# Kernel optimization log

Hardware: AMD Instinct MI355X
Metric: run time of the kernel (lower is better)

Reference implementation:

```python
import jax, jax.numpy as jnp
import numpy as np

WH, WW = 16, 16
NUM_HEADS = 16
DIM = 1024
BATCH = 64
SEQ = WH * WW + 1  # 257, includes cls token
NUM_REL = (2 * WH - 1) * (2 * WW - 1) + 3  # 964


def _make_rel_pos_index(wh, ww):
    # BEiT relative position index construction (intended semantics of the torch code)
    coords = np.stack(np.meshgrid(np.arange(wh), np.arange(ww), indexing='ij'))  # [2, wh, ww]
    flat = coords.reshape(2, -1)  # [2, wh*ww]
    rel = flat[:, :, None] - flat[:, None, :]  # [2, N-1, N-1]
    rel = rel.transpose(1, 2, 0).astype(np.int64)
    rel[:, :, 0] += wh - 1
    rel[:, :, 1] += ww - 1
    rel[:, :, 0] *= 2 * ww - 1
    num_rel = (2 * wh - 1) * (2 * ww - 1) + 3
    idx = np.zeros((wh * ww + 1, wh * ww + 1), dtype=np.int32)
    idx[1:, 1:] = rel.sum(-1)
    idx[0, :] = num_rel - 3  # cls-to-token
    idx[:, 0] = num_rel - 2  # token-to-cls
    idx[0, 0] = num_rel - 1  # cls-to-cls
    return idx


def setup_inputs() -> dict:
    key = jax.random.key(0)
    ks = jax.random.split(key, 7)
    return {
        'x': jax.random.normal(ks[0], (BATCH, SEQ, DIM), dtype=jnp.float32),
        'qkv_weight': jax.random.normal(ks[1], (3 * DIM, DIM), dtype=jnp.float32) * 0.02,
        'query_bias': jax.random.normal(ks[2], (DIM,), dtype=jnp.float32) * 0.02,
        'value_bias': jax.random.normal(ks[3], (DIM,), dtype=jnp.float32) * 0.02,
        'rel_pos_bias_table': jax.random.normal(ks[4], (NUM_REL, NUM_HEADS), dtype=jnp.float32) * 0.02,
        'proj_weight': jax.random.normal(ks[5], (DIM, DIM), dtype=jnp.float32) * 0.02,
        'proj_bias': jax.random.normal(ks[6], (DIM,), dtype=jnp.float32) * 0.02,
        'rel_pos_index': jnp.asarray(_make_rel_pos_index(WH, WW)),
    }


def reference(x, qkv_weight, query_bias, value_bias, rel_pos_bias_table,
              proj_weight, proj_bias, rel_pos_index):
    B, N, C = x.shape
    H = rel_pos_bias_table.shape[-1]
    D = qkv_weight.shape[0] // 3 // H
    scale = D ** -0.5
    # qkv bias: (q_bias, zeros, v_bias) as in the torch module
    qkv_bias = jnp.concatenate([query_bias, jnp.zeros_like(value_bias), value_bias])
    qkv = x @ qkv_weight.T + qkv_bias  # [B, N, 3*H*D]
    qkv = qkv.reshape(B, N, 3, H, D).transpose(2, 0, 3, 1, 4)  # [3, B, H, N, D]
    q, k, v = qkv[0] * scale, qkv[1], qkv[2]
    attn = jnp.einsum('bhqd,bhkd->bhqk', q, k)  # [B, H, N, N]
    bias = rel_pos_bias_table[rel_pos_index]  # [N, N, H]
    attn = attn + bias.transpose(2, 0, 1)[None]  # add per-head bias
    attn = jax.nn.softmax(attn, axis=-1)
    out = jnp.einsum('bhqk,bhkd->bhqd', attn, v)  # [B, H, N, D]
    out = out.transpose(0, 2, 1, 3).reshape(B, N, H * D)
    return out @ proj_weight.T + proj_bias
```

## Files before the change

kernel.cpp:

```cpp
#include <hip/hip_runtime.h>


typedef unsigned short u16;
typedef __attribute__((ext_vector_type(8))) short bf16x8;
typedef __attribute__((ext_vector_type(4))) float f32x4;

#define MFMA16(a, b, c) __builtin_amdgcn_mfma_f32_16x16x32_bf16(a, b, c, 0, 0, 0)
#define GLDS16(g, l)                                                           \
  __builtin_amdgcn_global_load_lds(                                            \
      (const __attribute__((address_space(1))) void*)(g),                      \
      (__attribute__((address_space(3))) void*)(l), 16, 0, 0)

#define QOFF 0
#define KOFF 16842752
#define VTOFF 33685504
#define VTP 264

__device__ __forceinline__ u16 f2bf(float f) {
  unsigned u = __builtin_bit_cast(unsigned, f);
  u += 0x7FFFu + ((u >> 16) & 1u);
  return (u16)(u >> 16);
}
__device__ __forceinline__ unsigned pack2(float a, float b) {
  return (unsigned)f2bf(a) | ((unsigned)f2bf(b) << 16);
}

__global__ __launch_bounds__(256) void cvt_bf16(const float* __restrict__ in,
                                                u16* __restrict__ out, int n4) {
  int i = blockIdx.x * 256 + threadIdx.x;
  if (i < n4) {
    float4 v = ((const float4*)in)[i];
    uint2 o;
    o.x = pack2(v.x, v.y);
    o.y = pack2(v.z, v.w);
    ((uint2*)out)[i] = o;
  }
}

__global__ __launch_bounds__(256) void bias_pre(const float* __restrict__ tab,
                                                const int* __restrict__ idx,
                                                float* __restrict__ out) {
  int t = blockIdx.x * 256 + threadIdx.x;
  if (t < 66049) {
    int id = idx[t];
    const float* row = tab + (size_t)id * 16;
#pragma unroll
    for (int h = 0; h < 16; h++)
      out[(size_t)h * 66049 + t] = row[h] * 1.4426950408889634f;
  }
}


#define GEMM_PROLOG(M_, K_)                                                    \
  __shared__ __align__(16) u16 SMEM[8192];                                     \
  u16* const As = SMEM;                                                        \
  u16* const Bs = SMEM + 4096;                                                 \
  const int M = (M_), K = (K_);                                                \
  const int tid = threadIdx.x;                                                 \
  const int lane = tid & 63, wave = tid >> 6;                                  \
  const int quad = lane >> 4, l15 = lane & 15;                                 \
  const int wr = (wave >> 1) * 64, wc = (wave & 1) * 64;                       \
  const int m0 = blockIdx.y * 128, n0 = blockIdx.x * 128;                      \
  const int sgk = (((tid & 3) ^ ((tid >> 3) & 3))) * 8;  \
  const int fo = ((quad ^ ((l15 >> 1) & 3))) * 8;         \
  int ar0 = m0 + (tid >> 2); if (ar0 > M - 1) ar0 = M - 1;                     \
  int ar1 = m0 + 64 + (tid >> 2); if (ar1 > M - 1) ar1 = M - 1;                \
  const u16* pa0 = A + (size_t)ar0 * K + sgk;                                  \
  const u16* pa1 = A + (size_t)ar1 * K + sgk;                                  \
  const u16* pb0 = B + (size_t)(n0 + (tid >> 2)) * K + sgk;                    \
  const u16* pb1 = pb0 + (size_t)64 * K;                                       \
  f32x4 acc[4][4];                                                             \
  _Pragma("unroll") for (int i = 0; i < 4; i++)                                \
  _Pragma("unroll") for (int j = 0; j < 4; j++)                                \
      acc[i][j] = (f32x4){0.f, 0.f, 0.f, 0.f};                                 \
  for (int k0 = 0; k0 < K; k0 += 32) {                                         \
    __syncthreads();                                                           \
    GLDS16(pa0 + k0, As + tid * 8);                                            \
    GLDS16(pa1 + k0, As + 2048 + tid * 8);                                     \
    GLDS16(pb0 + k0, Bs + tid * 8);                                            \
    GLDS16(pb1 + k0, Bs + 2048 + tid * 8);                                     \
    __syncthreads();                                                           \
    bf16x8 bfr[4];                                                             \
    _Pragma("unroll") for (int t = 0; t < 4; t++)                              \
        bfr[t] = *(const bf16x8*)(Bs + (wc + t * 16 + l15) * 32 + fo);         \
    _Pragma("unroll") for (int i = 0; i < 4; i++) {                            \
      bf16x8 afr = *(const bf16x8*)(As + (wr + i * 16 + l15) * 32 + fo);       \
      _Pragma("unroll") for (int j = 0; j < 4; j++)                            \
          acc[i][j] = MFMA16(afr, bfr[j], acc[i][j]);                          \
    }                                                                          \
  }

__global__ __launch_bounds__(256, 4) void gemm_qkv(
    const u16* __restrict__ A, const u16* __restrict__ B,
    const float* __restrict__ qbias, const float* __restrict__ vbias,
    u16* __restrict__ C) {
  GEMM_PROLOG(16448, 1024)
  if (n0 >= 2048) {
    u16* const T = SMEM;
    for (int p = 0; p < 2; p++) {
      __syncthreads();
      if ((wave & 1) == p) {
#pragma unroll
        for (int j = 0; j < 4; j++) {
          int cl = j * 16 + l15;
          int rem = (n0 + wc + j * 16 + l15) & 1023;
          float vb_ = vbias[rem];
          int swz = (cl & 15) << 3;
#pragma unroll
          for (int i = 0; i < 4; i++) {
            int rlb = wr + i * 16 + quad * 4;
#pragma unroll
            for (int rr = 0; rr < 2; rr++) {
              unsigned pk = pack2(acc[i][j][rr * 2] + vb_,
                                  acc[i][j][rr * 2 + 1] + vb_);
              *(unsigned*)(T + cl * 128 + ((rlb + rr * 2) ^ swz)) = pk;
            }
          }
        }
      }
      __syncthreads();
#pragma unroll
      for (int cc = 0; cc < 16; cc++) {
        int cl = cc * 4 + wave;
        int rem = (n0 + p * 64 + cl) & 1023;
        int h = rem >> 6, d = rem & 63;
        size_t cb = (size_t)VTOFF + ((size_t)h * 64 + d) * VTP;
        int swz = (cl & 15) << 3;
#pragma unroll
        for (int half = 0; half < 2; half++) {
          int rl = half * 64 + lane;
          u16 val = T[cl * 128 + (rl ^ swz)];
          int m = m0 + rl;
          if (m < M) {
            unsigned bb2 = (unsigned)m / 257u;
            unsigned nn2 = (unsigned)m - bb2 * 257u;
            C[cb + (size_t)bb2 * (16 * 64 * VTP) + nn2] = val;
          }
        }
      }
    }
  } else {
#pragma unroll
    for (int i = 0; i < 4; i++) {
#pragma unroll
      for (int r = 0; r < 4; r++) {
        int row = m0 + wr + i * 16 + quad * 4 + r;
        if (row < M) {
          unsigned bb = (unsigned)row / 257u;
          unsigned nn = (unsigned)row - bb * 257u;
#pragma unroll
          for (int j = 0; j < 4; j++) {
            int c = n0 + wc + j * 16 + l15;
            int which = c >> 10, rem = c & 1023;
            float bias = (which == 0) ? qbias[rem] : 0.f;
            float v = acc[i][j][r] + bias;
            if (which == 0) v *= 0.18033688011112042f;
            int h = rem >> 6, d = rem & 63;
            size_t dst = (size_t)which * 16842752 +
                         (size_t)(bb * 16 + h) * 16448 + (size_t)nn * 64 + d;
            C[dst] = f2bf(v);
          }
        }
      }
    }
  }
}

__global__ __launch_bounds__(256, 4) void gemm_proj(
    const u16* __restrict__ A, const u16* __restrict__ B,
    const float* __restrict__ pbias, float* __restrict__ C) {
  GEMM_PROLOG(16448, 1024)
#pragma unroll
  for (int i = 0; i < 4; i++) {
#pragma unroll
    for (int r = 0; r < 4; r++) {
      int row = m0 + wr + i * 16 + quad * 4 + r;
      if (row < M) {
#pragma unroll
        for (int j = 0; j < 4; j++) {
          int c = n0 + wc + j * 16 + l15;
          C[(size_t)row * 1024 + c] = acc[i][j][r] + pbias[c];
        }
      }
    }
  }
}

__global__ __launch_bounds__(256, 3) void attn_fused(
    const u16* __restrict__ qkv, const float* __restrict__ biasT,
    u16* __restrict__ out) {
  __shared__ __align__(16) u16 KVs[96 * 72];
  __shared__ __align__(16) u16 Ps[4 * 16 * 104];
  const int bx = blockIdx.x;
  const int qt = bx % 5, bh = bx / 5;
  const int b = bh >> 4, h = bh & 15;
  const int tid = threadIdx.x, lane = tid & 63, wave = tid >> 6;
  const int quad = lane >> 4, l15 = lane & 15;
  const u16* qg = qkv + QOFF + (size_t)bh * 16448;
  const u16* kg = qkv + KOFF + (size_t)bh * 16448;
  const u16* vtg = qkv + VTOFF + (size_t)bh * (64 * VTP);

  int qra = qt * 64 + wave * 16 + l15;
  if (qra > 256) qra = 256;
  const bf16x8 aq0 = *(const bf16x8*)(qg + (size_t)qra * 64 + quad * 8);
  const bf16x8 aq1 = *(const bf16x8*)(qg + (size_t)qra * 64 + 32 + quad * 8);

  const int qbase = qt * 64 + wave * 16 + quad * 4;
  const float* bb = biasT + (size_t)h * 66049;
  f32x4 s[18];
#pragma unroll
  for (int r = 0; r < 4; r++) {
    int qr = qbase + r;
    if (qr > 256) qr = 256;
    const float* brow = bb + (size_t)qr * 257;
#pragma unroll
    for (int t = 0; t < 18; t++) {
      int kc = t * 16 + l15;
      s[t][r] = (kc < 257) ? brow[kc] : -3e38f;
    }
  }

  const bf16x8 zv = {0, 0, 0, 0, 0, 0, 0, 0};
  for (int ck = 0; ck < 3; ck++) {
    __syncthreads();
#pragma unroll
    for (int it = 0; it < 3; it++) {
      int g = it * 256 + tid;
      int row = g >> 3, col = (g & 7) * 8;
      int gr = ck * 96 + row;
      bf16x8 kv = (gr < 257) ? *(const bf16x8*)(kg + (size_t)gr * 64 + col) : zv;
      *(bf16x8*)(KVs + row * 72 + col) = kv;
    }
    __syncthreads();
#pragma unroll
    for (int nt = 0; nt < 6; nt++) {
      bf16x8 b0 = *(const bf16x8*)(KVs + (nt * 16 + l15) * 72 + quad * 8);
      bf16x8 b1 = *(const bf16x8*)(KVs + (nt * 16 + l15) * 72 + 32 + quad * 8);
      int t = ck * 6 + nt;
      s[t] = MFMA16(aq0, b0, s[t]);
      s[t] = MFMA16(aq1, b1, s[t]);
    }
  }

  float inv[4];
#pragma unroll
  for (int r = 0; r < 4; r++) {
    float m = -3e38f;
#pragma unroll
    for (int t = 0; t < 18; t++) m = fmaxf(m, s[t][r]);
    m = fmaxf(m, __shfl_xor(m, 1));
    m = fmaxf(m, __shfl_xor(m, 2));
    m = fmaxf(m, __shfl_xor(m, 4));
    m = fmaxf(m, __shfl_xor(m, 8));
    float sum = 0.f;
#pragma unroll
    for (int t = 0; t < 18; t++) {
      float p = __builtin_amdgcn_exp2f(s[t][r] - m);
      s[t][r] = p;
      sum += p;
    }
    sum += __shfl_xor(sum, 1);
    sum += __shfl_xor(sum, 2);
    sum += __shfl_xor(sum, 4);
    sum += __shfl_xor(sum, 8);
    inv[r] = 1.f / sum;
  }

  u16* Pw = Ps + wave * (16 * 104);
  f32x4 o[4];
#pragma unroll
  for (int nt = 0; nt < 4; nt++) o[nt] = (f32x4){0.f, 0.f, 0.f, 0.f};
  for (int ck = 0; ck < 3; ck++) {
    __syncthreads();
#pragma unroll
    for (int it = 0; it < 3; it++) {
      int g = it * 256 + tid;
      int row = g / 12, c = (g % 12) * 8;
      bf16x8 v = *(const bf16x8*)(vtg + (size_t)row * VTP + ck * 96 + c);
      *(bf16x8*)(KVs + row * 104 + c) = v;
    }
#pragma unroll
    for (int nt = 0; nt < 6; nt++) {
      int t = ck * 6 + nt;
#pragma unroll
      for (int r = 0; r < 4; r++)
        Pw[(quad * 4 + r) * 104 + nt * 16 + l15] = f2bf(s[t][r]);
    }
    __syncthreads();
#pragma unroll
    for (int ks = 0; ks < 3; ks++) {
      bf16x8 ap = *(const bf16x8*)(Pw + l15 * 104 + ks * 32 + quad * 8);
#pragma unroll
      for (int nt = 0; nt < 4; nt++) {
        bf16x8 bv =
            *(const bf16x8*)(KVs + (nt * 16 + l15) * 104 + ks * 32 + quad * 8);
        o[nt] = MFMA16(ap, bv, o[nt]);
      }
    }
  }

#pragma unroll
  for (int nt = 0; nt < 4; nt++) {
    int d = nt * 16 + l15;
#pragma unroll
    for (int r = 0; r < 4; r++) {
      int qr = qbase + r;
      if (qr < 257)
        out[((size_t)b * 257 + qr) * 1024 + h * 64 + d] =
            f2bf(o[nt][r] * inv[r]);
    }
  }
}

extern "C" void kernel_launch(void* const* d_in, const int* in_sizes, int n_in,
                              void* d_out, int out_size, void* d_ws,
                              size_t ws_size, hipStream_t stream) {
  const float* x = (const float*)d_in[0];
  const float* qkvw = (const float*)d_in[1];
  const float* qb = (const float*)d_in[2];
  const float* vb = (const float*)d_in[3];
  const float* tab = (const float*)d_in[4];
  const float* pw = (const float*)d_in[5];
  const float* pb = (const float*)d_in[6];
  const int* rpi = (const int*)d_in[7];

  char* ws = (char*)d_ws;
  u16* qkvbuf = (u16*)ws;
  u16* xbuf = (u16*)(ws + 101974016);
  float* biasb = (float*)(ws + 135659520);
  u16* qkvwb = (u16*)(ws + 139886656);
  u16* projwb = (u16*)(ws + 146178112);

  cvt_bf16<<<16448, 256, 0, stream>>>(x, xbuf, 4210688);
  cvt_bf16<<<3072, 256, 0, stream>>>(qkvw, qkvwb, 786432);
  cvt_bf16<<<1024, 256, 0, stream>>>(pw, projwb, 262144);
  bias_pre<<<259, 256, 0, stream>>>(tab, rpi, biasb);
  gemm_qkv<<<dim3(24, 129), 256, 0, stream>>>(xbuf, qkvwb, qb, vb, qkvbuf);
  attn_fused<<<5120, 256, 0, stream>>>(qkvbuf, biasb, xbuf);
  gemm_proj<<<dim3(8, 129), 256, 0, stream>>>(xbuf, projwb, pb, (float*)d_out);
}
```

Baseline: 435.7 us.

## Triple-buffer GEMM K-loop with async global-to-LDS prefetch

Replaces the single-buffered, two-barrier K loop shared by the GEMM kernels with a three-stage LDS ring. Global-to-LDS loads for tile k+2 are issued while tile k is computed, and partial vmcnt waits keep loads in flight across iterations. It also drops the clamp on A row indices, which relies on A being padded or M being a multiple of 128, and hard-codes 32 K-steps, so K must be 1024. LDS per block triples to 48 KB, which may lower how many blocks fit per CU.

```diff
diff --git a/kernel.cpp b/kernel.cpp
--- a/kernel.cpp
+++ b/kernel.cpp
@@ -51,10 +51,28 @@
 }
 
 
+#define PIPE_STAGE(WRO, KS)                                                    \
+  GLDS16(pa0 + (KS), SMEM + (WRO) + tid * 8);                                  \
+  GLDS16(pa1 + (KS), SMEM + (WRO) + 2048 + tid * 8);                           \
+  GLDS16(pb0 + (KS), SMEM + (WRO) + 4096 + tid * 8);                           \
+  GLDS16(pb1 + (KS), SMEM + (WRO) + 6144 + tid * 8);
+
+#define PIPE_COMPUTE(RDO)                                                      \
+  {                                                                            \
+    const u16* As_ = SMEM + (RDO);                                             \
+    const u16* Bs_ = SMEM + (RDO) + 4096;                                      \
+    bf16x8 bfr[4];                                                             \
+    _Pragma("unroll") for (int t = 0; t < 4; t++)                              \
+        bfr[t] = *(const bf16x8*)(Bs_ + (wc + t * 16 + l15) * 32 + fo);        \
+    _Pragma("unroll") for (int i = 0; i < 4; i++) {                            \
+      bf16x8 afr = *(const bf16x8*)(As_ + (wr + i * 16 + l15) * 32 + fo);      \
+      _Pragma("unroll") for (int j = 0; j < 4; j++)                            \
+          acc[i][j] = MFMA16(afr, bfr[j], acc[i][j]);                          \
+    }                                                                          \
+  }
+
 #define GEMM_PROLOG(M_, K_)                                                    \
-  __shared__ __align__(16) u16 SMEM[8192];                                     \
-  u16* const As = SMEM;                                                        \
-  u16* const Bs = SMEM + 4096;                                                 \
+  __shared__ __align__(16) u16 SMEM[24576];               \
   const int M = (M_), K = (K_);                                                \
   const int tid = threadIdx.x;                                                 \
   const int lane = tid & 63, wave = tid >> 6;                                  \
@@ -63,32 +81,37 @@
   const int m0 = blockIdx.y * 128, n0 = blockIdx.x * 128;                      \
   const int sgk = (((tid & 3) ^ ((tid >> 3) & 3))) * 8;  \
   const int fo = ((quad ^ ((l15 >> 1) & 3))) * 8;         \
-  int ar0 = m0 + (tid >> 2); if (ar0 > M - 1) ar0 = M - 1;                     \
-  int ar1 = m0 + 64 + (tid >> 2); if (ar1 > M - 1) ar1 = M - 1;                \
-  const u16* pa0 = A + (size_t)ar0 * K + sgk;                                  \
-  const u16* pa1 = A + (size_t)ar1 * K + sgk;                                  \
+  const u16* pa0 = A + (size_t)(m0 + (tid >> 2)) * K + sgk;                    \
+  const u16* pa1 = pa0 + (size_t)64 * K;                                       \
   const u16* pb0 = B + (size_t)(n0 + (tid >> 2)) * K + sgk;                    \
   const u16* pb1 = pb0 + (size_t)64 * K;                                       \
   f32x4 acc[4][4];                                                             \
   _Pragma("unroll") for (int i = 0; i < 4; i++)                                \
   _Pragma("unroll") for (int j = 0; j < 4; j++)                                \
       acc[i][j] = (f32x4){0.f, 0.f, 0.f, 0.f};                                 \
-  for (int k0 = 0; k0 < K; k0 += 32) {                                         \
-    __syncthreads();                                                           \
-    GLDS16(pa0 + k0, As + tid * 8);                                            \
-    GLDS16(pa1 + k0, As + 2048 + tid * 8);                                     \
-    GLDS16(pb0 + k0, Bs + tid * 8);                                            \
-    GLDS16(pb1 + k0, Bs + 2048 + tid * 8);                                     \
-    __syncthreads();                                                           \
-    bf16x8 bfr[4];                                                             \
-    _Pragma("unroll") for (int t = 0; t < 4; t++)                              \
-        bfr[t] = *(const bf16x8*)(Bs + (wc + t * 16 + l15) * 32 + fo);         \
-    _Pragma("unroll") for (int i = 0; i < 4; i++) {                            \
-      bf16x8 afr = *(const bf16x8*)(As + (wr + i * 16 + l15) * 32 + fo);       \
-      _Pragma("unroll") for (int j = 0; j < 4; j++)                            \
-          acc[i][j] = MFMA16(afr, bfr[j], acc[i][j]);                          \
-    }                                                                          \
-  }
+  PIPE_STAGE(0, 0)                                                             \
+  PIPE_STAGE(8192, 32)                                                         \
+  int rdo = 0, wro = 16384;                                                    \
+  for (int it = 0; it < 30; ++it) {                                            \
+    PIPE_STAGE(wro, (it + 2) * 32)                                             \
+    asm volatile("s_waitcnt vmcnt(8)" ::: "memory");                           \
+    __builtin_amdgcn_s_barrier();                                              \
+    __builtin_amdgcn_sched_barrier(0);                                         \
+    PIPE_COMPUTE(rdo)                                                          \
+    asm volatile("s_waitcnt lgkmcnt(0)" ::: "memory");                         \
+    __builtin_amdgcn_s_barrier();                                              \
+    wro = rdo;                                                                 \
+    rdo = (rdo == 16384) ? 0 : rdo + 8192;                                     \
+  }                                                                            \
+  asm volatile("s_waitcnt vmcnt(4)" ::: "memory");                             \
+  __builtin_amdgcn_s_barrier();                                                \
+  __builtin_amdgcn_sched_barrier(0);                                           \
+  PIPE_COMPUTE(rdo)                                                            \
+  rdo = (rdo == 16384) ? 0 : rdo + 8192;                                       \
+  asm volatile("s_waitcnt vmcnt(0)" ::: "memory");                             \
+  __builtin_amdgcn_s_barrier();                                                \
+  __builtin_amdgcn_sched_barrier(0);                                           \
+  PIPE_COMPUTE(rdo)
 
 __global__ __launch_bounds__(256, 4) void gemm_qkv(
     const u16* __restrict__ A, const u16* __restrict__ B,
```

Result: slower. 527.4 us (+21.0%).
